# Performance work log

Measured on AMD Instinct MI355X. Metric: run time of the kernel, lower is better.

Reference implementation:

```python
import jax, jax.numpy as jnp
import numpy as np

N = 200000
E = 600000
H = 128
NUM_EDGE_TYPES = 16
LN_EPS = 1e-5


def setup_inputs() -> dict:
    key = jax.random.key(0)
    ks = jax.random.split(key, 10)
    x = jax.random.normal(ks[0], (N, H), dtype=jnp.float32)
    edge_index = jax.random.randint(ks[1], (2, E), 0, N, dtype=jnp.int32)
    edge_types = jax.random.randint(ks[2], (E,), 0, NUM_EDGE_TYPES, dtype=jnp.int32)
    s = 1.0 / np.sqrt(H)
    edge_emb = jax.random.normal(ks[3], (NUM_EDGE_TYPES, H), dtype=jnp.float32)
    W_self = jax.random.uniform(ks[4], (H, H), dtype=jnp.float32, minval=-s, maxval=s)
    b_self = jax.random.uniform(ks[5], (H,), dtype=jnp.float32, minval=-s, maxval=s)
    W_msg = jax.random.uniform(ks[6], (H, H), dtype=jnp.float32, minval=-s, maxval=s)
    b_msg = jax.random.uniform(ks[7], (H,), dtype=jnp.float32, minval=-s, maxval=s)
    gamma = jnp.ones((H,), dtype=jnp.float32)
    beta = jnp.zeros((H,), dtype=jnp.float32)
    return {
        "x": x, "edge_index": edge_index, "edge_types": edge_types,
        "edge_emb": edge_emb, "W_self": W_self, "b_self": b_self,
        "W_msg": W_msg, "b_msg": b_msg, "gamma": gamma, "beta": beta,
    }


def reference(x, edge_index, edge_types, edge_emb, W_self, b_self, W_msg, b_msg, gamma, beta):
    src = edge_index[0]
    dst = edge_index[1]
    # gather source node features + typed edge embedding: [E, H]
    typed_messages = x[src] + edge_emb[edge_types]
    # scatter-add into destination nodes: [N, H]
    aggregated = jnp.zeros_like(x).at[dst].add(typed_messages)
    # linear epilogue (torch Linear: y = x @ W.T + b)
    out = (x @ W_self.T + b_self) + (aggregated @ W_msg.T + b_msg)
    out = jax.nn.relu(out)
    # LayerNorm over last dim
    mu = jnp.mean(out, axis=-1, keepdims=True)
    var = jnp.mean(jnp.square(out - mu), axis=-1, keepdims=True)
    out = (out - mu) * jax.lax.rsqrt(var + LN_EPS) * gamma + beta
    # dropout is identity in eval mode
    return out
```

## Files before the change

kernel.cpp:

```cpp
#include <hip/hip_runtime.h>
#include <stdint.h>

#define H 128
#define TM 16
#define MAXDEG 24

typedef __attribute__((ext_vector_type(8))) short short8;
typedef __attribute__((ext_vector_type(4))) float f32x4;
typedef __attribute__((ext_vector_type(4))) int i32x4;

__device__ __forceinline__ unsigned short f2bf(float f) {
    union { float f; unsigned u; } v; v.f = f;
    unsigned u = v.u;
    u += 0x7fffu + ((u >> 16) & 1u);
    return (unsigned short)(u >> 16);
}

__device__ __forceinline__ float bf2f(unsigned short u) {
    union { unsigned u; float f; } v; v.u = ((unsigned)u) << 16; return v.f;
}

__device__ __forceinline__ short8 cvt8(f32x4 a, f32x4 b) {
    short8 r;
    r[0] = (short)f2bf(a.x); r[1] = (short)f2bf(a.y);
    r[2] = (short)f2bf(a.z); r[3] = (short)f2bf(a.w);
    r[4] = (short)f2bf(b.x); r[5] = (short)f2bf(b.y);
    r[6] = (short)f2bf(b.z); r[7] = (short)f2bf(b.w);
    return r;
}

__global__ __launch_bounds__(256) void prep_edges_kernel(
    const int* __restrict__ ei, const int* __restrict__ et,
    int* __restrict__ cnt, int* __restrict__ bucket, int E)
{
    int e = blockIdx.x * 256 + threadIdx.x;
    if (e >= E) return;
    int src = ei[e];
    int dst = ei[E + e];
    int t   = et[e];
    int pos = atomicAdd(&cnt[dst], 1);
    if (pos < MAXDEG) bucket[(size_t)dst * MAXDEG + pos] = src | (t << 18);
}

__global__ __launch_bounds__(256) void aggregate_kernel(
    const float* __restrict__ x, const float* __restrict__ emb,
    const int* __restrict__ cnt, const int* __restrict__ bucket,
    const int* __restrict__ ei, const int* __restrict__ et,
    unsigned short* __restrict__ aggb, int N, int E, int T)
{
    __shared__ __align__(16) float emb_s[16 * 132];

    const int tid = threadIdx.x;
    for (int i = tid; i < T * H; i += 256)
        emb_s[(i >> 7) * 132 + (i & 127)] = emb[i];
    __syncthreads();

    const int l = tid & 15;
    const int nGroups = N >> 4;

    for (int g = blockIdx.x; g < nGroups; g += gridDim.x) {
        const int node = (g << 4) + (tid >> 4);

        const int* b = bucket + (size_t)node * MAXDEG;
        i32x4 p = *(const i32x4*)b;
        const int c = cnt[node];

        f32x4 acc0 = {0.f, 0.f, 0.f, 0.f};
        f32x4 acc1 = {0.f, 0.f, 0.f, 0.f};

        if (c <= MAXDEG) {
            for (int i0 = 0; i0 < c; i0 += 4) {
                if (i0 > 0) p = *(const i32x4*)(b + i0);
                const int rem = c - i0;
                const bool h1 = rem > 1, h2 = rem > 2, h3 = rem > 3;

                f32x4 x00, x01, e00, e01, x10, x11, e10, e11;
                f32x4 x20, x21, e20, e21, x30, x31, e30, e31;
                {
                    int s = p.x & 0x3FFFF, t = p.x >> 18;
                    const float* xp = x + (size_t)s * H + l * 8;
                    const float* ep = emb_s + t * 132 + l * 8;
                    x00 = *(const f32x4*)xp;       x01 = *(const f32x4*)(xp + 4);
                    e00 = *(const f32x4*)ep;       e01 = *(const f32x4*)(ep + 4);
                }
                if (h1) {
                    int s = p.y & 0x3FFFF, t = p.y >> 18;
                    const float* xp = x + (size_t)s * H + l * 8;
                    const float* ep = emb_s + t * 132 + l * 8;
                    x10 = *(const f32x4*)xp;       x11 = *(const f32x4*)(xp + 4);
                    e10 = *(const f32x4*)ep;       e11 = *(const f32x4*)(ep + 4);
                }
                if (h2) {
                    int s = p.z & 0x3FFFF, t = p.z >> 18;
                    const float* xp = x + (size_t)s * H + l * 8;
                    const float* ep = emb_s + t * 132 + l * 8;
                    x20 = *(const f32x4*)xp;       x21 = *(const f32x4*)(xp + 4);
                    e20 = *(const f32x4*)ep;       e21 = *(const f32x4*)(ep + 4);
                }
                if (h3) {
                    int s = p.w & 0x3FFFF, t = p.w >> 18;
                    const float* xp = x + (size_t)s * H + l * 8;
                    const float* ep = emb_s + t * 132 + l * 8;
                    x30 = *(const f32x4*)xp;       x31 = *(const f32x4*)(xp + 4);
                    e30 = *(const f32x4*)ep;       e31 = *(const f32x4*)(ep + 4);
                }
                acc0 += x00 + e00;  acc1 += x01 + e01;
                if (h1) { acc0 += x10 + e10;  acc1 += x11 + e11; }
                if (h2) { acc0 += x20 + e20;  acc1 += x21 + e21; }
                if (h3) { acc0 += x30 + e30;  acc1 += x31 + e31; }
            }
        } else {
            for (int e = 0; e < E; ++e) {
                if (ei[E + e] == node) {
                    int s = ei[e], t = et[e];
                    const float* xp = x + (size_t)s * H + l * 8;
                    const float* ep = emb_s + t * 132 + l * 8;
                    f32x4 v0 = *(const f32x4*)xp, v1 = *(const f32x4*)(xp + 4);
                    f32x4 w0 = *(const f32x4*)ep, w1 = *(const f32x4*)(ep + 4);
                    acc0 += v0 + w0;  acc1 += v1 + w1;
                }
            }
        }

        *(short8*)(aggb + (size_t)node * H + l * 8) = cvt8(acc0, acc1);
    }
}

__global__ __launch_bounds__(256) void gemm_ln_kernel(
    const float* __restrict__ x, const unsigned short* __restrict__ aggb,
    const float* __restrict__ Wself, const float* __restrict__ bself,
    const float* __restrict__ Wmsg, const float* __restrict__ bmsg,
    const float* __restrict__ gamma, const float* __restrict__ beta,
    float* __restrict__ out, int nTiles)
{
    __shared__ __align__(16) short a_stage[TM * 264];
    __shared__ __align__(16) float o_stage[TM * 132];

    const int tid  = threadIdx.x;
    const int wave = tid >> 6;
    const int lane = tid & 63;
    const int col  = lane & 15;
    const int quad = lane >> 4;

    short8 bfrag[2][8];
    float bias[2];
#pragma unroll
    for (int s = 0; s < 2; ++s) {
        const int h = (wave * 2 + s) * 16 + col;
        bias[s] = bself[h] + bmsg[h];
#pragma unroll
        for (int kst = 0; kst < 8; ++kst) {
            const float* W = (kst < 4) ? Wself : Wmsg;
            const int k0 = (kst & 3) * 32 + quad * 8;
            const float* p = W + (size_t)h * H + k0;
            f32x4 w0 = *(const f32x4*)(p);
            f32x4 w1 = *(const f32x4*)(p + 4);
            bfrag[s][kst] = cvt8(w0, w1);
        }
    }

    const int lnode = tid >> 4;
    const int f0 = (tid & 15) * 8;
    f32x4 g0  = *(const f32x4*)(gamma + f0);
    f32x4 g1  = *(const f32x4*)(gamma + f0 + 4);
    f32x4 be0 = *(const f32x4*)(beta + f0);
    f32x4 be1 = *(const f32x4*)(beta + f0 + 4);

    const int node = tid >> 4;
    const int seg  = tid & 15;

    for (int tile = blockIdx.x; tile < nTiles; tile += gridDim.x) {
        const size_t rowBase = (size_t)tile * TM;

        if (seg < 8) {
            const float* src = x + (rowBase + node) * H + seg * 16;
            f32x4 v0 = ((const f32x4*)src)[0];
            f32x4 v1 = ((const f32x4*)src)[1];
            f32x4 v2 = ((const f32x4*)src)[2];
            f32x4 v3 = ((const f32x4*)src)[3];
            *(short8*)&a_stage[node * 264 + seg * 16]     = cvt8(v0, v1);
            *(short8*)&a_stage[node * 264 + seg * 16 + 8] = cvt8(v2, v3);
        } else {
            const unsigned short* src = aggb + (rowBase + node) * H + (seg - 8) * 16;
            *(short8*)&a_stage[node * 264 + 128 + (seg - 8) * 16]     = *(const short8*)src;
            *(short8*)&a_stage[node * 264 + 128 + (seg - 8) * 16 + 8] = *(const short8*)(src + 8);
        }
        __syncthreads();

        short8 afr[8];
#pragma unroll
        for (int kst = 0; kst < 8; ++kst)
            afr[kst] = *(const short8*)(&a_stage[col * 264 + kst * 32 + quad * 8]);

        f32x4 acc0 = {0.f, 0.f, 0.f, 0.f};
        f32x4 acc1 = {0.f, 0.f, 0.f, 0.f};
#pragma unroll
        for (int kst = 0; kst < 8; ++kst) {
            acc0 = __builtin_amdgcn_mfma_f32_16x16x32_bf16(afr[kst], bfrag[0][kst], acc0, 0, 0, 0);
            acc1 = __builtin_amdgcn_mfma_f32_16x16x32_bf16(afr[kst], bfrag[1][kst], acc1, 0, 0, 0);
        }

#pragma unroll
        for (int s = 0; s < 2; ++s) {
            const int h = (wave * 2 + s) * 16 + col;
            f32x4 a = s ? acc1 : acc0;
#pragma unroll
            for (int r = 0; r < 4; ++r) {
                const int m = quad * 4 + r;
                float v = a[r] + bias[s];
                o_stage[m * 132 + h] = v > 0.f ? v : 0.f;
            }
        }
        __syncthreads();

        float v[8];
        float s1 = 0.f, s2 = 0.f;
#pragma unroll
        for (int j = 0; j < 8; ++j) {
            v[j] = o_stage[lnode * 132 + f0 + j];
            s1 += v[j];
            s2 += v[j] * v[j];
        }
#pragma unroll
        for (int m = 1; m < 16; m <<= 1) {
            s1 += __shfl_xor(s1, m, 64);
            s2 += __shfl_xor(s2, m, 64);
        }
        const float mu = s1 * (1.f / 128.f);
        const float var = s2 * (1.f / 128.f) - mu * mu;
        const float rstd = rsqrtf(var + 1e-5f);

        f32x4 o0, o1;
        o0.x = (v[0] - mu) * rstd * g0.x + be0.x;
        o0.y = (v[1] - mu) * rstd * g0.y + be0.y;
        o0.z = (v[2] - mu) * rstd * g0.z + be0.z;
        o0.w = (v[3] - mu) * rstd * g0.w + be0.w;
        o1.x = (v[4] - mu) * rstd * g1.x + be1.x;
        o1.y = (v[5] - mu) * rstd * g1.y + be1.y;
        o1.z = (v[6] - mu) * rstd * g1.z + be1.z;
        o1.w = (v[7] - mu) * rstd * g1.w + be1.w;

        float* dst = out + (rowBase + lnode) * H + f0;
        __builtin_nontemporal_store(o0, (f32x4*)dst);
        __builtin_nontemporal_store(o1, (f32x4*)(dst + 4));
    }
}

__global__ __launch_bounds__(256) void scatter_kernel(
    const float* __restrict__ x, const int* __restrict__ ei,
    const int* __restrict__ et, const float* __restrict__ emb,
    float* __restrict__ agg, int E)
{
    int g = blockIdx.x * 256 + threadIdx.x;
    int e = g >> 5;
    int l = g & 31;
    if (e >= E) return;
    int src = ei[e];
    int dst = ei[E + e];
    int t   = et[e];
    f32x4 xv = *(const f32x4*)(x   + (size_t)src * H + l * 4);
    f32x4 ev = *(const f32x4*)(emb + (size_t)t   * H + l * 4);
    float* b = agg + (size_t)dst * H + l * 4;
    atomicAdd(b + 0, xv.x + ev.x);
    atomicAdd(b + 1, xv.y + ev.y);
    atomicAdd(b + 2, xv.z + ev.z);
    atomicAdd(b + 3, xv.w + ev.w);
}

__global__ __launch_bounds__(256) void gemm_ln_f32_kernel(
    const float* __restrict__ x,
    const float* __restrict__ Wself, const float* __restrict__ bself,
    const float* __restrict__ Wmsg, const float* __restrict__ bmsg,
    const float* __restrict__ gamma, const float* __restrict__ beta,
    float* __restrict__ out, int nTiles)
{
    __shared__ __align__(16) short a_stage[TM * 264];
    __shared__ __align__(16) float o_stage[TM * 132];

    const int tid  = threadIdx.x;
    const int wave = tid >> 6;
    const int lane = tid & 63;
    const int col  = lane & 15;
    const int quad = lane >> 4;

    short8 bfrag[2][8];
    float bias[2];
#pragma unroll
    for (int s = 0; s < 2; ++s) {
        const int h = (wave * 2 + s) * 16 + col;
        bias[s] = bself[h] + bmsg[h];
#pragma unroll
        for (int kst = 0; kst < 8; ++kst) {
            const float* W = (kst < 4) ? Wself : Wmsg;
            const int k0 = (kst & 3) * 32 + quad * 8;
            const float* p = W + (size_t)h * H + k0;
            f32x4 w0 = *(const f32x4*)(p);
            f32x4 w1 = *(const f32x4*)(p + 4);
            bfrag[s][kst] = cvt8(w0, w1);
        }
    }

    const int lnode = tid >> 4;
    const int f0 = (tid & 15) * 8;
    f32x4 g0  = *(const f32x4*)(gamma + f0);
    f32x4 g1  = *(const f32x4*)(gamma + f0 + 4);
    f32x4 be0 = *(const f32x4*)(beta + f0);
    f32x4 be1 = *(const f32x4*)(beta + f0 + 4);

    for (int tile = blockIdx.x; tile < nTiles; tile += gridDim.x) {
        const size_t rowBase = (size_t)tile * TM;
        {
            const int node = tid >> 4;
            const int seg  = tid & 15;
            const int k0   = seg * 16;
            const float* src = (seg < 8)
                ? (x   + (rowBase + node) * H + k0)
                : (out + (rowBase + node) * H + (k0 - 128));
            f32x4 v0 = ((const f32x4*)src)[0];
            f32x4 v1 = ((const f32x4*)src)[1];
            f32x4 v2 = ((const f32x4*)src)[2];
            f32x4 v3 = ((const f32x4*)src)[3];
            *(short8*)(&a_stage[node * 264 + k0])     = cvt8(v0, v1);
            *(short8*)(&a_stage[node * 264 + k0 + 8]) = cvt8(v2, v3);
        }
        __syncthreads();

        short8 afr[8];
#pragma unroll
        for (int kst = 0; kst < 8; ++kst)
            afr[kst] = *(const short8*)(&a_stage[col * 264 + kst * 32 + quad * 8]);

        f32x4 acc0 = {0.f, 0.f, 0.f, 0.f};
        f32x4 acc1 = {0.f, 0.f, 0.f, 0.f};
#pragma unroll
        for (int kst = 0; kst < 8; ++kst) {
            acc0 = __builtin_amdgcn_mfma_f32_16x16x32_bf16(afr[kst], bfrag[0][kst], acc0, 0, 0, 0);
            acc1 = __builtin_amdgcn_mfma_f32_16x16x32_bf16(afr[kst], bfrag[1][kst], acc1, 0, 0, 0);
        }

#pragma unroll
        for (int s = 0; s < 2; ++s) {
            const int h = (wave * 2 + s) * 16 + col;
            f32x4 a = s ? acc1 : acc0;
#pragma unroll
            for (int r = 0; r < 4; ++r) {
                const int m = quad * 4 + r;
                float v = a[r] + bias[s];
                o_stage[m * 132 + h] = v > 0.f ? v : 0.f;
            }
        }
        __syncthreads();

        float v[8];
        float s1 = 0.f, s2 = 0.f;
#pragma unroll
        for (int j = 0; j < 8; ++j) {
            v[j] = o_stage[lnode * 132 + f0 + j];
            s1 += v[j];
            s2 += v[j] * v[j];
        }
#pragma unroll
        for (int m = 1; m < 16; m <<= 1) {
            s1 += __shfl_xor(s1, m, 64);
            s2 += __shfl_xor(s2, m, 64);
        }
        const float mu = s1 * (1.f / 128.f);
        const float var = s2 * (1.f / 128.f) - mu * mu;
        const float rstd = rsqrtf(var + 1e-5f);

        f32x4 o0, o1;
        o0.x = (v[0] - mu) * rstd * g0.x + be0.x;
        o0.y = (v[1] - mu) * rstd * g0.y + be0.y;
        o0.z = (v[2] - mu) * rstd * g0.z + be0.z;
        o0.w = (v[3] - mu) * rstd * g0.w + be0.w;
        o1.x = (v[4] - mu) * rstd * g1.x + be1.x;
        o1.y = (v[5] - mu) * rstd * g1.y + be1.y;
        o1.z = (v[6] - mu) * rstd * g1.z + be1.z;
        o1.w = (v[7] - mu) * rstd * g1.w + be1.w;

        float* dst = out + (rowBase + lnode) * H + f0;
        *(f32x4*)(dst)     = o0;
        *(f32x4*)(dst + 4) = o1;
    }
}

extern "C" void kernel_launch(void* const* d_in, const int* in_sizes, int n_in,
                              void* d_out, int out_size, void* d_ws, size_t ws_size,
                              hipStream_t stream) {
    const float* x     = (const float*)d_in[0];
    const int*   ei    = (const int*)d_in[1];
    const int*   et    = (const int*)d_in[2];
    const float* emb   = (const float*)d_in[3];
    const float* Wself = (const float*)d_in[4];
    const float* bself = (const float*)d_in[5];
    const float* Wmsg  = (const float*)d_in[6];
    const float* bmsg  = (const float*)d_in[7];
    const float* gamma = (const float*)d_in[8];
    const float* beta  = (const float*)d_in[9];
    float* out = (float*)d_out;

    const int E = in_sizes[2];
    const int N = in_sizes[0] / H;
    const int T = in_sizes[3] / H;
    const int nTiles = N / TM;

    auto rnd = [](size_t b) { return (b + 255) & ~(size_t)255; };
    const size_t sz_agg = rnd((size_t)N * H * 2);
    const size_t sz_cnt = rnd((size_t)N * 4);
    const size_t sz_bkt = rnd((size_t)N * MAXDEG * 4);
    const size_t needA = sz_agg + sz_cnt + sz_bkt;

    const bool tierA = (ws_size >= needA) && (N <= (1 << 18)) && (T <= 16)
                       && (N % TM == 0);

    if (tierA) {
        uint8_t* p = (uint8_t*)d_ws;
        unsigned short* aggb = (unsigned short*)p;  p += sz_agg;
        int* cnt    = (int*)p;                      p += sz_cnt;
        int* bucket = (int*)p;

        hipMemsetAsync(cnt, 0, (size_t)N * sizeof(int), stream);

        if (E > 0) {
            prep_edges_kernel<<<(E + 255) / 256, 256, 0, stream>>>(
                ei, et, cnt, bucket, E);
        }

        const int nGroups = N >> 4;
        int aggGrid = nGroups < 4096 ? nGroups : 4096;
        aggregate_kernel<<<aggGrid, 256, 0, stream>>>(
            x, emb, cnt, bucket, ei, et, aggb, N, E, T);

        int gemmGrid = nTiles < 2048 ? nTiles : 2048;
        gemm_ln_kernel<<<gemmGrid, 256, 0, stream>>>(
            x, aggb, Wself, bself, Wmsg, bmsg, gamma, beta, out, nTiles);
    } else {
        hipMemsetAsync(out, 0, (size_t)N * H * sizeof(float), stream);
        const long long sthreads = (long long)E * 32;
        scatter_kernel<<<(int)((sthreads + 255) / 256), 256, 0, stream>>>(
            x, ei, et, emb, out, E);
        int grid = 2500;
        if (grid > nTiles) grid = nTiles;
        gemm_ln_f32_kernel<<<grid, 256, 0, stream>>>(
            x, Wself, bself, Wmsg, bmsg, gamma, beta, out, nTiles);
    }
}
```

Baseline: 338.4 us.

## Pre-convert x to bf16 for gather and GEMM, fuse prep, use 32-row GEMM tiles

Adds a prep kernel that converts x and the edge embeddings to bf16 and builds the dst buckets in the same launch. The aggregation then gathers half-width bf16 rows instead of fp32 rows. A new GEMM+LayerNorm kernel reads the bf16 x, processes 32 rows per iteration, keeps gamma/beta in LDS and writes the output with nontemporal stores. The cost is an extra full pass over x to write the bf16 copy, plus the rounding error of bf16 inputs accumulated in the aggregation.

```diff
diff --git a/kernel.cpp b/kernel.cpp
--- a/kernel.cpp
+++ b/kernel.cpp
@@ -27,6 +27,33 @@
     r[4] = (short)f2bf(b.x); r[5] = (short)f2bf(b.y);
     r[6] = (short)f2bf(b.z); r[7] = (short)f2bf(b.w);
     return r;
+}
+
+__global__ __launch_bounds__(256) void prep_kernel(
+    const float* __restrict__ x, const float* __restrict__ emb,
+    unsigned short* __restrict__ xb, unsigned short* __restrict__ embb,
+    const int* __restrict__ ei, const int* __restrict__ et,
+    int* __restrict__ cnt, int* __restrict__ bucket,
+    int total8x, int total8e, int E)
+{
+    int i = blockIdx.x * 256 + threadIdx.x;
+    if (i < total8x) {
+        f32x4 a = ((const f32x4*)x)[2 * i];
+        f32x4 b = ((const f32x4*)x)[2 * i + 1];
+        ((short8*)xb)[i] = cvt8(a, b);
+    } else if (i < total8x + total8e) {
+        int j = i - total8x;
+        f32x4 a = ((const f32x4*)emb)[2 * j];
+        f32x4 b = ((const f32x4*)emb)[2 * j + 1];
+        ((short8*)embb)[j] = cvt8(a, b);
+    }
+    if (i < E) {
+        int src = ei[i];
+        int dst = ei[E + i];
+        int t   = et[i];
+        int pos = atomicAdd(&cnt[dst], 1);
+        if (pos < MAXDEG) bucket[(size_t)dst * MAXDEG + pos] = src | (t << 18);
+    }
 }
 
 __global__ __launch_bounds__(256) void prep_edges_kernel(
@@ -42,7 +69,230 @@
     if (pos < MAXDEG) bucket[(size_t)dst * MAXDEG + pos] = src | (t << 18);
 }
 
-__global__ __launch_bounds__(256) void aggregate_kernel(
+__global__ __launch_bounds__(256) void aggregate_bf16_kernel(
+    const unsigned short* __restrict__ xb, const unsigned short* __restrict__ embb,
+    const int* __restrict__ cnt, const int* __restrict__ bucket,
+    const int* __restrict__ ei, const int* __restrict__ et,
+    unsigned short* __restrict__ aggb, int N, int E, int T)
+{
+    __shared__ __align__(16) short emb_s[16 * 136];
+
+    const int tid = threadIdx.x;
+    const int l   = tid & 15;
+    if (tid < T * 16) {
+        int t = tid >> 4;
+        *(short8*)&emb_s[t * 136 + l * 8] = *(const short8*)(embb + t * H + l * 8);
+    }
+    __syncthreads();
+
+    const int nGroups = N >> 4;
+    for (int g = blockIdx.x; g < nGroups; g += gridDim.x) {
+        const int node = (g << 4) + (tid >> 4);
+
+        const int* b = bucket + (size_t)node * MAXDEG;
+        i32x4 p = *(const i32x4*)b;
+        const int c = cnt[node];
+
+        float acc[8] = {0.f, 0.f, 0.f, 0.f, 0.f, 0.f, 0.f, 0.f};
+
+        if (c <= MAXDEG) {
+            for (int i0 = 0; i0 < c; i0 += 4) {
+                if (i0 > 0) p = *(const i32x4*)(b + i0);
+                const int rem = c - i0;
+                const bool h1 = rem > 1, h2 = rem > 2, h3 = rem > 3;
+                short8 xv0, xv1, xv2, xv3, ev0, ev1, ev2, ev3;
+                {
+                    int s = p.x & 0x3FFFF, t = p.x >> 18;
+                    xv0 = *(const short8*)(xb + (size_t)s * H + l * 8);
+                    ev0 = *(const short8*)&emb_s[t * 136 + l * 8];
+                }
+                if (h1) {
+                    int s = p.y & 0x3FFFF, t = p.y >> 18;
+                    xv1 = *(const short8*)(xb + (size_t)s * H + l * 8);
+                    ev1 = *(const short8*)&emb_s[t * 136 + l * 8];
+                }
+                if (h2) {
+                    int s = p.z & 0x3FFFF, t = p.z >> 18;
+                    xv2 = *(const short8*)(xb + (size_t)s * H + l * 8);
+                    ev2 = *(const short8*)&emb_s[t * 136 + l * 8];
+                }
+                if (h3) {
+                    int s = p.w & 0x3FFFF, t = p.w >> 18;
+                    xv3 = *(const short8*)(xb + (size_t)s * H + l * 8);
+                    ev3 = *(const short8*)&emb_s[t * 136 + l * 8];
+                }
+#pragma unroll
+                for (int j = 0; j < 8; ++j) acc[j] += bf2f((unsigned short)xv0[j]) + bf2f((unsigned short)ev0[j]);
+                if (h1) {
+#pragma unroll
+                    for (int j = 0; j < 8; ++j) acc[j] += bf2f((unsigned short)xv1[j]) + bf2f((unsigned short)ev1[j]);
+                }
+                if (h2) {
+#pragma unroll
+                    for (int j = 0; j < 8; ++j) acc[j] += bf2f((unsigned short)xv2[j]) + bf2f((unsigned short)ev2[j]);
+                }
+                if (h3) {
+#pragma unroll
+                    for (int j = 0; j < 8; ++j) acc[j] += bf2f((unsigned short)xv3[j]) + bf2f((unsigned short)ev3[j]);
+                }
+            }
+        } else {
+            for (int e = 0; e < E; ++e) {
+                if (ei[E + e] == node) {
+                    int s = ei[e], t = et[e];
+                    short8 xv = *(const short8*)(xb + (size_t)s * H + l * 8);
+                    short8 ev = *(const short8*)&emb_s[t * 136 + l * 8];
+#pragma unroll
+                    for (int j = 0; j < 8; ++j) acc[j] += bf2f((unsigned short)xv[j]) + bf2f((unsigned short)ev[j]);
+                }
+            }
+        }
+
+        short8 r;
+#pragma unroll
+        for (int j = 0; j < 8; ++j) r[j] = (short)f2bf(acc[j]);
+        *(short8*)(aggb + (size_t)node * H + l * 8) = r;
+    }
+}
+
+__global__ __launch_bounds__(256) void gemm_ln32_kernel(
+    const unsigned short* __restrict__ xb, const unsigned short* __restrict__ aggb,
+    const float* __restrict__ Wself, const float* __restrict__ bself,
+    const float* __restrict__ Wmsg, const float* __restrict__ bmsg,
+    const float* __restrict__ gamma, const float* __restrict__ beta,
+    float* __restrict__ out, int nSuper)
+{
+    __shared__ __align__(16) short a_stage[32 * 264];
+    __shared__ __align__(16) float o_stage[32 * 132];
+    __shared__ __align__(16) float gb_s[256];
+
+    const int tid  = threadIdx.x;
+    const int wave = tid >> 6;
+    const int lane = tid & 63;
+    const int col  = lane & 15;
+    const int quad = lane >> 4;
+
+    if (tid < 128) gb_s[tid] = gamma[tid];
+    else           gb_s[tid] = beta[tid - 128];
+
+    short8 bfrag[2][8];
+    float bias[2];
+#pragma unroll
+    for (int s = 0; s < 2; ++s) {
+        const int h = (wave * 2 + s) * 16 + col;
+        bias[s] = bself[h] + bmsg[h];
+#pragma unroll
+        for (int kst = 0; kst < 8; ++kst) {
+            const float* W = (kst < 4) ? Wself : Wmsg;
+            const int k0 = (kst & 3) * 32 + quad * 8;
+            const float* p = W + (size_t)h * H + k0;
+            bfrag[s][kst] = cvt8(*(const f32x4*)p, *(const f32x4*)(p + 4));
+        }
+    }
+
+    const int srow = tid >> 3;
+    const int sq   = tid & 7;
+
+    __syncthreads();
+
+    for (int st = blockIdx.x; st < nSuper; st += gridDim.x) {
+        const size_t rowBase = (size_t)st * 32;
+
+        {
+            const unsigned short* src = (sq < 4)
+                ? (xb   + (rowBase + srow) * H + sq * 32)
+                : (aggb + (rowBase + srow) * H + (sq - 4) * 32);
+            short* dstl = &a_stage[srow * 264 + (sq & 3) * 32 + ((sq >> 2) << 7)];
+            *(short8*)(dstl)      = ((const short8*)src)[0];
+            *(short8*)(dstl + 8)  = ((const short8*)src)[1];
+            *(short8*)(dstl + 16) = ((const short8*)src)[2];
+            *(short8*)(dstl + 24) = ((const short8*)src)[3];
+        }
+        __syncthreads();
+
+        f32x4 acc00 = {0.f,0.f,0.f,0.f}, acc01 = {0.f,0.f,0.f,0.f};
+        f32x4 acc10 = {0.f,0.f,0.f,0.f}, acc11 = {0.f,0.f,0.f,0.f};
+        {
+            short8 afr[8];
+#pragma unroll
+            for (int kst = 0; kst < 8; ++kst)
+                afr[kst] = *(const short8*)&a_stage[col * 264 + kst * 32 + quad * 8];
+#pragma unroll
+            for (int kst = 0; kst < 8; ++kst) {
+                acc00 = __builtin_amdgcn_mfma_f32_16x16x32_bf16(afr[kst], bfrag[0][kst], acc00, 0, 0, 0);
+                acc01 = __builtin_amdgcn_mfma_f32_16x16x32_bf16(afr[kst], bfrag[1][kst], acc01, 0, 0, 0);
+            }
+#pragma unroll
+            for (int kst = 0; kst < 8; ++kst)
+                afr[kst] = *(const short8*)&a_stage[(16 + col) * 264 + kst * 32 + quad * 8];
+#pragma unroll
+            for (int kst = 0; kst < 8; ++kst) {
+                acc10 = __builtin_amdgcn_mfma_f32_16x16x32_bf16(afr[kst], bfrag[0][kst], acc10, 0, 0, 0);
+                acc11 = __builtin_amdgcn_mfma_f32_16x16x32_bf16(afr[kst], bfrag[1][kst], acc11, 0, 0, 0);
+            }
+        }
+
+        {
+            const int h0 = (wave * 2) * 16 + col;
+            const int h1 = h0 + 16;
+#pragma unroll
+            for (int r = 0; r < 4; ++r) {
+                const int m = quad * 4 + r;
+                float v;
+                v = acc00[r] + bias[0]; o_stage[m * 132 + h0]        = v > 0.f ? v : 0.f;
+                v = acc01[r] + bias[1]; o_stage[m * 132 + h1]        = v > 0.f ? v : 0.f;
+                v = acc10[r] + bias[0]; o_stage[(16 + m) * 132 + h0] = v > 0.f ? v : 0.f;
+                v = acc11[r] + bias[1]; o_stage[(16 + m) * 132 + h1] = v > 0.f ? v : 0.f;
+            }
+        }
+        __syncthreads();
+
+        const float* orow = &o_stage[srow * 132 + sq * 16];
+        f32x4 v0 = ((const f32x4*)orow)[0];
+        f32x4 v1 = ((const f32x4*)orow)[1];
+        f32x4 v2 = ((const f32x4*)orow)[2];
+        f32x4 v3 = ((const f32x4*)orow)[3];
+
+        float s1 = (v0.x + v0.y + v0.z + v0.w) + (v1.x + v1.y + v1.z + v1.w)
+                 + (v2.x + v2.y + v2.z + v2.w) + (v3.x + v3.y + v3.z + v3.w);
+        float s2 = v0.x*v0.x + v0.y*v0.y + v0.z*v0.z + v0.w*v0.w
+                 + v1.x*v1.x + v1.y*v1.y + v1.z*v1.z + v1.w*v1.w
+                 + v2.x*v2.x + v2.y*v2.y + v2.z*v2.z + v2.w*v2.w
+                 + v3.x*v3.x + v3.y*v3.y + v3.z*v3.z + v3.w*v3.w;
+#pragma unroll
+        for (int m = 1; m < 8; m <<= 1) {
+            s1 += __shfl_xor(s1, m, 64);
+            s2 += __shfl_xor(s2, m, 64);
+        }
+        const float mu = s1 * (1.f / 128.f);
+        const float var = s2 * (1.f / 128.f) - mu * mu;
+        const float rstd = rsqrtf(var + 1e-5f);
+
+        float* dst = out + (rowBase + srow) * H + sq * 16;
+        {
+            f32x4 gg, be, o;
+            gg = *(const f32x4*)&gb_s[sq * 16 + 0];  be = *(const f32x4*)&gb_s[128 + sq * 16 + 0];
+            o.x = (v0.x - mu) * rstd * gg.x + be.x;  o.y = (v0.y - mu) * rstd * gg.y + be.y;
+            o.z = (v0.z - mu) * rstd * gg.z + be.z;  o.w = (v0.w - mu) * rstd * gg.w + be.w;
+            __builtin_nontemporal_store(o, (f32x4*)(dst + 0));
+            gg = *(const f32x4*)&gb_s[sq * 16 + 4];  be = *(const f32x4*)&gb_s[128 + sq * 16 + 4];
+            o.x = (v1.x - mu) * rstd * gg.x + be.x;  o.y = (v1.y - mu) * rstd * gg.y + be.y;
+            o.z = (v1.z - mu) * rstd * gg.z + be.z;  o.w = (v1.w - mu) * rstd * gg.w + be.w;
+            __builtin_nontemporal_store(o, (f32x4*)(dst + 4));
+            gg = *(const f32x4*)&gb_s[sq * 16 + 8];  be = *(const f32x4*)&gb_s[128 + sq * 16 + 8];
+            o.x = (v2.x - mu) * rstd * gg.x + be.x;  o.y = (v2.y - mu) * rstd * gg.y + be.y;
+            o.z = (v2.z - mu) * rstd * gg.z + be.z;  o.w = (v2.w - mu) * rstd * gg.w + be.w;
+            __builtin_nontemporal_store(o, (f32x4*)(dst + 8));
+            gg = *(const f32x4*)&gb_s[sq * 16 + 12]; be = *(const f32x4*)&gb_s[128 + sq * 16 + 12];
+            o.x = (v3.x - mu) * rstd * gg.x + be.x;  o.y = (v3.y - mu) * rstd * gg.y + be.y;
+            o.z = (v3.z - mu) * rstd * gg.z + be.z;  o.w = (v3.w - mu) * rstd * gg.w + be.w;
+            __builtin_nontemporal_store(o, (f32x4*)(dst + 12));
+        }
+        __syncthreads();
+    }
+}
+
+__global__ __launch_bounds__(256) void aggregate_f32_kernel(
     const float* __restrict__ x, const float* __restrict__ emb,
     const int* __restrict__ cnt, const int* __restrict__ bucket,
     const int* __restrict__ ei, const int* __restrict__ et,
@@ -60,49 +310,46 @@
 
     for (int g = blockIdx.x; g < nGroups; g += gridDim.x) {
         const int node = (g << 4) + (tid >> 4);
-
         const int* b = bucket + (size_t)node * MAXDEG;
         i32x4 p = *(const i32x4*)b;
         const int c = cnt[node];
 
-        f32x4 acc0 = {0.f, 0.f, 0.f, 0.f};
-        f32x4 acc1 = {0.f, 0.f, 0.f, 0.f};
+        f32x4 acc0 = {0.f,0.f,0.f,0.f};
+        f32x4 acc1 = {0.f,0.f,0.f,0.f};
 
         if (c <= MAXDEG) {
             for (int i0 = 0; i0 < c; i0 += 4) {
                 if (i0 > 0) p = *(const i32x4*)(b + i0);
                 const int rem = c - i0;
                 const bool h1 = rem > 1, h2 = rem > 2, h3 = rem > 3;
-
-                f32x4 x00, x01, e00, e01, x10, x11, e10, e11;
-                f32x4 x20, x21, e20, e21, x30, x31, e30, e31;
+                f32x4 x00,x01,e00,e01,x10,x11,e10,e11,x20,x21,e20,e21,x30,x31,e30,e31;
                 {
                     int s = p.x & 0x3FFFF, t = p.x >> 18;
                     const float* xp = x + (size_t)s * H + l * 8;
                     const float* ep = emb_s + t * 132 + l * 8;
-                    x00 = *(const f32x4*)xp;       x01 = *(const f32x4*)(xp + 4);
-                    e00 = *(const f32x4*)ep;       e01 = *(const f32x4*)(ep + 4);
+                    x00 = *(const f32x4*)xp; x01 = *(const f32x4*)(xp + 4);
+                    e00 = *(const f32x4*)ep; e01 = *(const f32x4*)(ep + 4);
                 }
                 if (h1) {
                     int s = p.y & 0x3FFFF, t = p.y >> 18;
                     const float* xp = x + (size_t)s * H + l * 8;
                     const float* ep = emb_s + t * 132 + l * 8;
-                    x10 = *(const f32x4*)xp;       x11 = *(const f32x4*)(xp + 4);
-                    e10 = *(const f32x4*)ep;       e11 = *(const f32x4*)(ep + 4);
+                    x10 = *(const f32x4*)xp; x11 = *(const f32x4*)(xp + 4);
+                    e10 = *(const f32x4*)ep; e11 = *(const f32x4*)(ep + 4);
                 }
                 if (h2) {
                     int s = p.z & 0x3FFFF, t = p.z >> 18;
                     const float* xp = x + (size_t)s * H + l * 8;
                     const float* ep = emb_s + t * 132 + l * 8;
-                    x20 = *(const f32x4*)xp;       x21 = *(const f32x4*)(xp + 4);
-                    e20 = *(const f32x4*)ep;       e21 = *(const f32x4*)(ep + 4);
+                    x20 = *(const f32x4*)xp; x21 = *(const f32x4*)(xp + 4);
+                    e20 = *(const f32x4*)ep; e21 = *(const f32x4*)(ep + 4);
                 }
                 if (h3) {
                     int s = p.w & 0x3FFFF, t = p.w >> 18;
                     const float* xp = x + (size_t)s * H + l * 8;
                     const float* ep = emb_s + t * 132 + l * 8;
-                    x30 = *(const f32x4*)xp;       x31 = *(const f32x4*)(xp + 4);
-                    e30 = *(const f32x4*)ep;       e31 = *(const f32x4*)(ep + 4);
+                    x30 = *(const f32x4*)xp; x31 = *(const f32x4*)(xp + 4);
+                    e30 = *(const f32x4*)ep; e31 = *(const f32x4*)(ep + 4);
                 }
                 acc0 += x00 + e00;  acc1 += x01 + e01;
                 if (h1) { acc0 += x10 + e10;  acc1 += x11 + e11; }
@@ -115,18 +362,17 @@
                     int s = ei[e], t = et[e];
                     const float* xp = x + (size_t)s * H + l * 8;
                     const float* ep = emb_s + t * 132 + l * 8;
-                    f32x4 v0 = *(const f32x4*)xp, v1 = *(const f32x4*)(xp + 4);
-                    f32x4 w0 = *(const f32x4*)ep, w1 = *(const f32x4*)(ep + 4);
-                    acc0 += v0 + w0;  acc1 += v1 + w1;
-                }
-            }
-        }
-
+                    f32x4 a0 = *(const f32x4*)xp, a1 = *(const f32x4*)(xp + 4);
+                    f32x4 b0 = *(const f32x4*)ep, b1 = *(const f32x4*)(ep + 4);
+                    acc0 += a0 + b0;  acc1 += a1 + b1;
+                }
+            }
+        }
         *(short8*)(aggb + (size_t)node * H + l * 8) = cvt8(acc0, acc1);
     }
 }
 
-__global__ __launch_bounds__(256) void gemm_ln_kernel(
+__global__ __launch_bounds__(256) void gemm_ln16_kernel(
     const float* __restrict__ x, const unsigned short* __restrict__ aggb,
     const float* __restrict__ Wself, const float* __restrict__ bself,
     const float* __restrict__ Wmsg, const float* __restrict__ bmsg,
@@ -153,9 +399,7 @@
             const float* W = (kst < 4) ? Wself : Wmsg;
             const int k0 = (kst & 3) * 32 + quad * 8;
             const float* p = W + (size_t)h * H + k0;
-            f32x4 w0 = *(const f32x4*)(p);
-            f32x4 w1 = *(const f32x4*)(p + 4);
-            bfrag[s][kst] = cvt8(w0, w1);
+            bfrag[s][kst] = cvt8(*(const f32x4*)p, *(const f32x4*)(p + 4));
         }
     }
 
@@ -171,7 +415,6 @@
 
     for (int tile = blockIdx.x; tile < nTiles; tile += gridDim.x) {
         const size_t rowBase = (size_t)tile * TM;
-
         if (seg < 8) {
             const float* src = x + (rowBase + node) * H + seg * 16;
             f32x4 v0 = ((const f32x4*)src)[0];
@@ -192,8 +435,8 @@
         for (int kst = 0; kst < 8; ++kst)
             afr[kst] = *(const short8*)(&a_stage[col * 264 + kst * 32 + quad * 8]);
 
-        f32x4 acc0 = {0.f, 0.f, 0.f, 0.f};
-        f32x4 acc1 = {0.f, 0.f, 0.f, 0.f};
+        f32x4 acc0 = {0.f,0.f,0.f,0.f};
+        f32x4 acc1 = {0.f,0.f,0.f,0.f};
 #pragma unroll
         for (int kst = 0; kst < 8; ++kst) {
             acc0 = __builtin_amdgcn_mfma_f32_16x16x32_bf16(afr[kst], bfrag[0][kst], acc0, 0, 0, 0);
@@ -294,9 +537,7 @@
             const float* W = (kst < 4) ? Wself : Wmsg;
             const int k0 = (kst & 3) * 32 + quad * 8;
             const float* p = W + (size_t)h * H + k0;
-            f32x4 w0 = *(const f32x4*)(p);
-            f32x4 w1 = *(const f32x4*)(p + 4);
-            bfrag[s][kst] = cvt8(w0, w1);
+            bfrag[s][kst] = cvt8(*(const f32x4*)p, *(const f32x4*)(p + 4));
         }
     }
 
@@ -330,8 +571,8 @@
         for (int kst = 0; kst < 8; ++kst)
             afr[kst] = *(const short8*)(&a_stage[col * 264 + kst * 32 + quad * 8]);
 
-        f32x4 acc0 = {0.f, 0.f, 0.f, 0.f};
-        f32x4 acc1 = {0.f, 0.f, 0.f, 0.f};
+        f32x4 acc0 = {0.f,0.f,0.f,0.f};
+        f32x4 acc1 = {0.f,0.f,0.f,0.f};
 #pragma unroll
         for (int kst = 0; kst < 8; ++kst) {
             acc0 = __builtin_amdgcn_mfma_f32_16x16x32_bf16(afr[kst], bfrag[0][kst], acc0, 0, 0, 0);
@@ -405,15 +646,43 @@
     const int nTiles = N / TM;
 
     auto rnd = [](size_t b) { return (b + 255) & ~(size_t)255; };
-    const size_t sz_agg = rnd((size_t)N * H * 2);
-    const size_t sz_cnt = rnd((size_t)N * 4);
-    const size_t sz_bkt = rnd((size_t)N * MAXDEG * 4);
-    const size_t needA = sz_agg + sz_cnt + sz_bkt;
-
-    const bool tierA = (ws_size >= needA) && (N <= (1 << 18)) && (T <= 16)
-                       && (N % TM == 0);
+    const size_t sz_xb   = rnd((size_t)N * H * 2);
+    const size_t sz_embb = rnd((size_t)T * H * 2);
+    const size_t sz_agg  = rnd((size_t)N * H * 2);
+    const size_t sz_cnt  = rnd((size_t)N * 4);
+    const size_t sz_bkt  = rnd((size_t)N * MAXDEG * 4);
+    const size_t needA = sz_xb + sz_embb + sz_agg + sz_cnt + sz_bkt;
+    const size_t needB = sz_agg + sz_cnt + sz_bkt;
+
+    const bool okT = (T <= 16) && (N <= (1 << 18));
+    const bool tierA = okT && (ws_size >= needA) && (N % 32 == 0);
+    const bool tierB = okT && (ws_size >= needB) && (N % TM == 0);
 
     if (tierA) {
+        uint8_t* p = (uint8_t*)d_ws;
+        unsigned short* xb   = (unsigned short*)p;  p += sz_xb;
+        unsigned short* embb = (unsigned short*)p;  p += sz_embb;
+        unsigned short* aggb = (unsigned short*)p;  p += sz_agg;
+        int* cnt    = (int*)p;                      p += sz_cnt;
+        int* bucket = (int*)p;
+
+        hipMemsetAsync(cnt, 0, (size_t)N * sizeof(int), stream);
+
+        const int t8x = N * H / 8, t8e = T * H / 8;
+        int prepWork = (t8x + t8e) > E ? (t8x + t8e) : E;
+        prep_kernel<<<(prepWork + 255) / 256, 256, 0, stream>>>(
+            x, emb, xb, embb, ei, et, cnt, bucket, t8x, t8e, E);
+
+        const int nGroups = N >> 4;
+        int aggGrid = nGroups < 6250 ? nGroups : 6250;
+        aggregate_bf16_kernel<<<aggGrid, 256, 0, stream>>>(
+            xb, embb, cnt, bucket, ei, et, aggb, N, E, T);
+
+        const int nSuper = N / 32;
+        int gemmGrid = nSuper < 3125 ? nSuper : 3125;
+        gemm_ln32_kernel<<<gemmGrid, 256, 0, stream>>>(
+            xb, aggb, Wself, bself, Wmsg, bmsg, gamma, beta, out, nSuper);
+    } else if (tierB) {
         uint8_t* p = (uint8_t*)d_ws;
         unsigned short* aggb = (unsigned short*)p;  p += sz_agg;
         int* cnt    = (int*)p;                      p += sz_cnt;
@@ -425,14 +694,13 @@
             prep_edges_kernel<<<(E + 255) / 256, 256, 0, stream>>>(
                 ei, et, cnt, bucket, E);
         }
-
         const int nGroups = N >> 4;
         int aggGrid = nGroups < 4096 ? nGroups : 4096;
-        aggregate_kernel<<<aggGrid, 256, 0, stream>>>(
+        aggregate_f32_kernel<<<aggGrid, 256, 0, stream>>>(
             x, emb, cnt, bucket, ei, et, aggb, N, E, T);
 
         int gemmGrid = nTiles < 2048 ? nTiles : 2048;
-        gemm_ln_kernel<<<gemmGrid, 256, 0, stream>>>(
+        gemm_ln16_kernel<<<gemmGrid, 256, 0, stream>>>(
             x, aggb, Wself, bself, Wmsg, bmsg, gamma, beta, out, nTiles);
     } else {
         hipMemsetAsync(out, 0, (size_t)N * H * sizeof(float), stream);
```

Measured after the change: 411.2 us. 21.5% more time.
